# Performance work log

Hardware: AMD Instinct MI355X
Metric: run time of the kernel (lower is better)

The kernel has to match this reference:

```python
import jax, jax.numpy as jnp
import numpy as np

B, IN_CH, OUT_CH, N_MAPS, H, W_DIM, CTRL = 64, 32, 32, 64, 64, 64, 512
NF = N_MAPS                # forget gate units
NI = IN_CH * N_MAPS       # input gate units
NO = OUT_CH * N_MAPS      # output gate units


def setup_inputs() -> dict:
    key = jax.random.key(0)
    k1, k2, k3, k4 = jax.random.split(key, 4)
    inputs = jax.random.normal(k1, (B, IN_CH, H, W_DIM), dtype=jnp.float32)
    state = jax.random.normal(k2, (B, N_MAPS, H, W_DIM), dtype=jnp.float32)
    controls = jax.random.normal(k3, (B, CTRL), dtype=jnp.float32)
    Wc = jax.random.normal(k4, (NF + NI + NO, CTRL), dtype=jnp.float32) * (CTRL ** -0.5)
    return {"inputs": inputs, "state": state, "controls": controls, "W": Wc}


def reference(inputs, state, controls, W):
    # control linear (no bias): [B, NF+NI+NO]
    ctrl = controls @ W.T
    f = ctrl[:, :NF]                         # [B, n_maps]
    i = ctrl[:, NF:NF + NI]                  # [B, in_ch*n_maps]
    o = ctrl[:, NF + NI:]                    # [B, out_ch*n_maps]
    in_gates = i.reshape(B, N_MAPS, IN_CH)   # per-sample 1x1 conv filters
    forget_gates = f.reshape(B, N_MAPS, 1, 1)
    out_gates = o.reshape(B, OUT_CH, N_MAPS)
    # per-sample 1x1 conv == batched channel contraction
    gated_inputs = jnp.einsum('bchw,bmc->bmhw', inputs, in_gates)
    new_state = gated_inputs + state * forget_gates
    output = jnp.tanh(new_state)
    outputs = jnp.einsum('bmhw,bom->bohw', output, out_gates)
    return (outputs, new_state)
```

## Files before the change

kernel.cpp:

```cpp
#include <hip/hip_runtime.h>
#include <cstdint>
#include <cstddef>

#define B_SZ   64
#define IN_CH  32
#define OUT_CH 32
#define NMAPS  64
#define HW     4096
#define CTRLN  512
#define NROWS  4160
#define OUT0_SZ (B_SZ*OUT_CH*HW)
#define TILE   128

typedef short bf8_t  __attribute__((ext_vector_type(8)));
typedef float f32x4  __attribute__((ext_vector_type(4)));

__device__ __forceinline__ unsigned short f2bf(float f) {
    union { float f; uint32_t u; } v; v.f = f;
    return (unsigned short)((v.u + 0x7FFFu + ((v.u >> 16) & 1u)) >> 16);
}
__device__ __forceinline__ float fast_tanh(float x) {
    float e = __expf(2.0f * x);
    return 1.0f - 2.0f * __builtin_amdgcn_rcpf(e + 1.0f);
}

__global__ __launch_bounds__(256) void ctrl_gemm(
    const float* __restrict__ controls, const float* __restrict__ W,
    float* __restrict__ ws)
{
    __shared__ __align__(16) float ct[128 * 65];
    const int tid = threadIdx.x;
    const int b   = tid & 63;
    const int w   = __builtin_amdgcn_readfirstlane(tid >> 6);
    const int j0  = blockIdx.x * 16 + w * 4;
    const float* w0 = W + (size_t)j0 * CTRLN;

    float acc[4] = {0.f, 0.f, 0.f, 0.f};
    for (int kc = 0; kc < CTRLN; kc += 128) {
        __syncthreads();
#pragma unroll
        for (int i = 0; i < 8; ++i) {
            const int flat = (i * 256 + tid) * 4;
            const int bb = flat >> 7;
            const int kk = flat & 127;
            float4 v = *(const float4*)(controls + (size_t)bb * CTRLN + kc + kk);
            ct[(kk + 0) * 65 + bb] = v.x;
            ct[(kk + 1) * 65 + bb] = v.y;
            ct[(kk + 2) * 65 + bb] = v.z;
            ct[(kk + 3) * 65 + bb] = v.w;
        }
        __syncthreads();
#pragma unroll 4
        for (int k = 0; k < 128; ++k) {
            const float c = ct[k * 65 + b];
#pragma unroll
            for (int r = 0; r < 4; ++r)
                acc[r] += w0[r * CTRLN + kc + k] * c;
        }
    }
    float* wb = ws + (size_t)b * NROWS + j0;
#pragma unroll
    for (int r = 0; r < 4; ++r) wb[r] = acc[r];
}

__global__ __launch_bounds__(256, 4) void vstm_main(
    const float* __restrict__ inputs, const float* __restrict__ state,
    const float* __restrict__ ws, float* __restrict__ out)
{
    __shared__ __align__(16) unsigned short Xt[TILE * 40];
    __shared__ __align__(16) unsigned short IGs[64 * 40];
    __shared__ __align__(16) unsigned short OGs[32 * 72];
    __shared__ __align__(16) unsigned short Tt[TILE * 72];
    __shared__ __align__(16) float fs[64];

    const int tid  = threadIdx.x;
    const int b    = blockIdx.y;
    const int tile = blockIdx.x * TILE;
    const int w    = __builtin_amdgcn_readfirstlane(tid >> 6);
    const int l    = tid & 63;
    const int lhi  = l >> 4;
    const int llo  = l & 15;

    const float* g = ws + (size_t)b * NROWS;
    if (tid < 64) fs[tid] = g[tid];
#pragma unroll
    for (int i = 0; i < 8; ++i) {
        const int idx = i * 256 + tid;
        IGs[(idx >> 5) * 40 + (idx & 31)] = f2bf(g[64 + idx]);
        OGs[(idx >> 6) * 72 + (idx & 63)] = f2bf(g[2112 + idx]);
    }
    const float* inb = inputs + (size_t)b * IN_CH * HW + tile;
#pragma unroll
    for (int i = 0; i < 16; ++i) {
        const int flat = i * 256 + tid;
        const int c = flat >> 7, p = flat & 127;
        Xt[p * 40 + c] = f2bf(inb[c * HW + p]);
    }
    __syncthreads();

    const bf8_t af = *(const bf8_t*)&IGs[(w * 16 + llo) * 40 + lhi * 8];
    f32x4 acc[8];
#pragma unroll
    for (int pc = 0; pc < 8; ++pc) {
        acc[pc] = (f32x4){0.f, 0.f, 0.f, 0.f};
        const bf8_t bf = *(const bf8_t*)&Xt[(pc * 16 + llo) * 40 + lhi * 8];
        acc[pc] = __builtin_amdgcn_mfma_f32_16x16x32_bf16(af, bf, acc[pc], 0, 0, 0);
    }

    float fr[4];
#pragma unroll
    for (int r = 0; r < 4; ++r) fr[r] = fs[w * 16 + lhi * 4 + r];

    const float* stb = state + (size_t)b * NMAPS * HW + tile;
    float*       nsb = out + OUT0_SZ + (size_t)b * NMAPS * HW + tile;
#pragma unroll
    for (int pc = 0; pc < 8; ++pc) {
        const int p = pc * 16 + llo;
#pragma unroll
        for (int r = 0; r < 4; ++r) {
            const int m = w * 16 + lhi * 4 + r;
            const float ns = acc[pc][r] + stb[m * HW + p] * fr[r];
            nsb[m * HW + p] = ns;
            Tt[p * 72 + m] = f2bf(fast_tanh(ns));
        }
    }
    __syncthreads();

    const int oc  = w >> 1;
    const int pcb = (w & 1) * 4;
    bf8_t ag[2];
#pragma unroll
    for (int ks = 0; ks < 2; ++ks)
        ag[ks] = *(const bf8_t*)&OGs[(oc * 16 + llo) * 72 + ks * 32 + lhi * 8];

    f32x4 acc2[4];
#pragma unroll
    for (int t = 0; t < 4; ++t) {
        acc2[t] = (f32x4){0.f, 0.f, 0.f, 0.f};
        const int pc = pcb + t;
#pragma unroll
        for (int ks = 0; ks < 2; ++ks) {
            const bf8_t bt = *(const bf8_t*)&Tt[(pc * 16 + llo) * 72 + ks * 32 + lhi * 8];
            acc2[t] = __builtin_amdgcn_mfma_f32_16x16x32_bf16(ag[ks], bt, acc2[t], 0, 0, 0);
        }
    }

    float* ob = out + (size_t)b * OUT_CH * HW + tile;
#pragma unroll
    for (int t = 0; t < 4; ++t) {
        const int p = (pcb + t) * 16 + llo;
#pragma unroll
        for (int r = 0; r < 4; ++r) {
            const int o = oc * 16 + lhi * 4 + r;
            ob[o * HW + p] = acc2[t][r];
        }
    }
}

extern "C" void kernel_launch(void* const* d_in, const int* in_sizes, int n_in,
                              void* d_out, int out_size, void* d_ws, size_t ws_size,
                              hipStream_t stream) {
    const float* inputs   = (const float*)d_in[0];
    const float* state    = (const float*)d_in[1];
    const float* controls = (const float*)d_in[2];
    const float* W        = (const float*)d_in[3];
    float*       out      = (float*)d_out;
    float*       ws       = (float*)d_ws;

    ctrl_gemm<<<dim3(NROWS / 16), 256, 0, stream>>>(controls, W, ws);

    dim3 g2(HW / TILE, B_SZ);
    vstm_main<<<g2, 256, 0, stream>>>(inputs, state, ws, out);
}
```

Before: 227.8 us.

## Swap MFMA operand roles so each wave owns pixel rows and uses float4 state and output I/O

The main kernel swaps the MFMA A and B operands so each wave owns a 32-pixel slice across all maps. The accumulator rows then map to consecutive pixels, which lets state loads, new_state stores and output stores use float4 accesses. Because each wave only reads back its own Tt rows, the barrier between the tanh store and the second GEMM is removed. Gate staging is also vectorized to float4 loads, and the control GEMM is split into twice as many blocks with two rows per wave to raise parallelism. Removing the barrier relies on the same wave writing and then reading those Tt rows, and the transposed Tt stores stay scalar and may cause LDS bank conflicts.

```diff
diff --git a/kernel.cpp b/kernel.cpp
--- a/kernel.cpp
+++ b/kernel.cpp
@@ -13,6 +13,7 @@
 #define TILE   128
 
 typedef short bf8_t  __attribute__((ext_vector_type(8)));
+typedef short bf4_t  __attribute__((ext_vector_type(4)));
 typedef float f32x4  __attribute__((ext_vector_type(4)));
 
 __device__ __forceinline__ unsigned short f2bf(float f) {
@@ -32,10 +33,10 @@
     const int tid = threadIdx.x;
     const int b   = tid & 63;
     const int w   = __builtin_amdgcn_readfirstlane(tid >> 6);
-    const int j0  = blockIdx.x * 16 + w * 4;
+    const int j0  = blockIdx.x * 8 + w * 2;
     const float* w0 = W + (size_t)j0 * CTRLN;
 
-    float acc[4] = {0.f, 0.f, 0.f, 0.f};
+    float acc0 = 0.f, acc1 = 0.f;
     for (int kc = 0; kc < CTRLN; kc += 128) {
         __syncthreads();
 #pragma unroll
@@ -50,17 +51,15 @@
             ct[(kk + 3) * 65 + bb] = v.w;
         }
         __syncthreads();
-#pragma unroll 4
+#pragma unroll 8
         for (int k = 0; k < 128; ++k) {
             const float c = ct[k * 65 + b];
-#pragma unroll
-            for (int r = 0; r < 4; ++r)
-                acc[r] += w0[r * CTRLN + kc + k] * c;
-        }
-    }
-    float* wb = ws + (size_t)b * NROWS + j0;
-#pragma unroll
-    for (int r = 0; r < 4; ++r) wb[r] = acc[r];
+            acc0 += w0[kc + k] * c;
+            acc1 += w0[CTRLN + kc + k] * c;
+        }
+    }
+    ws[(size_t)b * NROWS + j0]     = acc0;
+    ws[(size_t)b * NROWS + j0 + 1] = acc1;
 }
 
 __global__ __launch_bounds__(256, 4) void vstm_main(
@@ -78,16 +77,22 @@
     const int tile = blockIdx.x * TILE;
     const int w    = __builtin_amdgcn_readfirstlane(tid >> 6);
     const int l    = tid & 63;
-    const int lhi  = l >> 4;
-    const int llo  = l & 15;
+    const int quad = l >> 4;
+    const int mlo  = l & 15;
 
     const float* g = ws + (size_t)b * NROWS;
     if (tid < 64) fs[tid] = g[tid];
 #pragma unroll
-    for (int i = 0; i < 8; ++i) {
-        const int idx = i * 256 + tid;
-        IGs[(idx >> 5) * 40 + (idx & 31)] = f2bf(g[64 + idx]);
-        OGs[(idx >> 6) * 72 + (idx & 63)] = f2bf(g[2112 + idx]);
+    for (int i = 0; i < 2; ++i) {
+        const int e = (i * 256 + tid) * 4;
+        float4 gi = *(const float4*)(g + 64 + e);
+        bf4_t vi = { (short)f2bf(gi.x), (short)f2bf(gi.y),
+                     (short)f2bf(gi.z), (short)f2bf(gi.w) };
+        *(bf4_t*)&IGs[(e >> 5) * 40 + (e & 31)] = vi;
+        float4 go = *(const float4*)(g + 2112 + e);
+        bf4_t vo = { (short)f2bf(go.x), (short)f2bf(go.y),
+                     (short)f2bf(go.z), (short)f2bf(go.w) };
+        *(bf4_t*)&OGs[(e >> 6) * 72 + (e & 63)] = vo;
     }
     const float* inb = inputs + (size_t)b * IN_CH * HW + tile;
 #pragma unroll
@@ -98,63 +103,85 @@
     }
     __syncthreads();
 
-    const bf8_t af = *(const bf8_t*)&IGs[(w * 16 + llo) * 40 + lhi * 8];
-    f32x4 acc[8];
-#pragma unroll
-    for (int pc = 0; pc < 8; ++pc) {
-        acc[pc] = (f32x4){0.f, 0.f, 0.f, 0.f};
-        const bf8_t bf = *(const bf8_t*)&Xt[(pc * 16 + llo) * 40 + lhi * 8];
-        acc[pc] = __builtin_amdgcn_mfma_f32_16x16x32_bf16(af, bf, acc[pc], 0, 0, 0);
-    }
-
-    float fr[4];
-#pragma unroll
-    for (int r = 0; r < 4; ++r) fr[r] = fs[w * 16 + lhi * 4 + r];
+    bf8_t af[2], bg[4];
+#pragma unroll
+    for (int pc = 0; pc < 2; ++pc)
+        af[pc] = *(const bf8_t*)&Xt[(w * 32 + pc * 16 + mlo) * 40 + quad * 8];
+#pragma unroll
+    for (int mc = 0; mc < 4; ++mc)
+        bg[mc] = *(const bf8_t*)&IGs[(mc * 16 + mlo) * 40 + quad * 8];
+
+    f32x4 acc[2][4];
+#pragma unroll
+    for (int pc = 0; pc < 2; ++pc)
+#pragma unroll
+        for (int mc = 0; mc < 4; ++mc) {
+            acc[pc][mc] = (f32x4){0.f, 0.f, 0.f, 0.f};
+            acc[pc][mc] = __builtin_amdgcn_mfma_f32_16x16x32_bf16(
+                af[pc], bg[mc], acc[pc][mc], 0, 0, 0);
+        }
 
     const float* stb = state + (size_t)b * NMAPS * HW + tile;
     float*       nsb = out + OUT0_SZ + (size_t)b * NMAPS * HW + tile;
 #pragma unroll
-    for (int pc = 0; pc < 8; ++pc) {
-        const int p = pc * 16 + llo;
-#pragma unroll
-        for (int r = 0; r < 4; ++r) {
-            const int m = w * 16 + lhi * 4 + r;
-            const float ns = acc[pc][r] + stb[m * HW + p] * fr[r];
-            nsb[m * HW + p] = ns;
-            Tt[p * 72 + m] = f2bf(fast_tanh(ns));
-        }
-    }
-    __syncthreads();
-
-    const int oc  = w >> 1;
-    const int pcb = (w & 1) * 4;
-    bf8_t ag[2];
-#pragma unroll
-    for (int ks = 0; ks < 2; ++ks)
-        ag[ks] = *(const bf8_t*)&OGs[(oc * 16 + llo) * 72 + ks * 32 + lhi * 8];
-
-    f32x4 acc2[4];
-#pragma unroll
-    for (int t = 0; t < 4; ++t) {
-        acc2[t] = (f32x4){0.f, 0.f, 0.f, 0.f};
-        const int pc = pcb + t;
-#pragma unroll
-        for (int ks = 0; ks < 2; ++ks) {
-            const bf8_t bt = *(const bf8_t*)&Tt[(pc * 16 + llo) * 72 + ks * 32 + lhi * 8];
-            acc2[t] = __builtin_amdgcn_mfma_f32_16x16x32_bf16(ag[ks], bt, acc2[t], 0, 0, 0);
-        }
-    }
+    for (int mc = 0; mc < 4; ++mc) {
+        const int m = mc * 16 + mlo;
+        const float fgt = fs[m];
+#pragma unroll
+        for (int pc = 0; pc < 2; ++pc) {
+            const int p0 = w * 32 + pc * 16 + quad * 4;
+            const float4 st = *(const float4*)(stb + (size_t)m * HW + p0);
+            float4 ns;
+            ns.x = acc[pc][mc][0] + st.x * fgt;
+            ns.y = acc[pc][mc][1] + st.y * fgt;
+            ns.z = acc[pc][mc][2] + st.z * fgt;
+            ns.w = acc[pc][mc][3] + st.w * fgt;
+            *(float4*)(nsb + (size_t)m * HW + p0) = ns;
+            Tt[(p0 + 0) * 72 + m] = f2bf(fast_tanh(ns.x));
+            Tt[(p0 + 1) * 72 + m] = f2bf(fast_tanh(ns.y));
+            Tt[(p0 + 2) * 72 + m] = f2bf(fast_tanh(ns.z));
+            Tt[(p0 + 3) * 72 + m] = f2bf(fast_tanh(ns.w));
+        }
+    }
+
+    bf8_t ag[2][2], at[2][2];
+#pragma unroll
+    for (int oc = 0; oc < 2; ++oc)
+#pragma unroll
+        for (int ks = 0; ks < 2; ++ks)
+            ag[oc][ks] = *(const bf8_t*)&OGs[(oc * 16 + mlo) * 72 + ks * 32 + quad * 8];
+#pragma unroll
+    for (int pc = 0; pc < 2; ++pc)
+#pragma unroll
+        for (int ks = 0; ks < 2; ++ks)
+            at[pc][ks] = *(const bf8_t*)&Tt[(w * 32 + pc * 16 + mlo) * 72 + ks * 32 + quad * 8];
+
+    f32x4 acc2[2][2];
+#pragma unroll
+    for (int pc = 0; pc < 2; ++pc)
+#pragma unroll
+        for (int oc = 0; oc < 2; ++oc) {
+            acc2[pc][oc] = (f32x4){0.f, 0.f, 0.f, 0.f};
+#pragma unroll
+            for (int ks = 0; ks < 2; ++ks)
+                acc2[pc][oc] = __builtin_amdgcn_mfma_f32_16x16x32_bf16(
+                    at[pc][ks], ag[oc][ks], acc2[pc][oc], 0, 0, 0);
+        }
 
     float* ob = out + (size_t)b * OUT_CH * HW + tile;
 #pragma unroll
-    for (int t = 0; t < 4; ++t) {
-        const int p = (pcb + t) * 16 + llo;
-#pragma unroll
-        for (int r = 0; r < 4; ++r) {
-            const int o = oc * 16 + lhi * 4 + r;
-            ob[o * HW + p] = acc2[t][r];
-        }
-    }
+    for (int pc = 0; pc < 2; ++pc)
+#pragma unroll
+        for (int oc = 0; oc < 2; ++oc) {
+            const int p0 = w * 32 + pc * 16 + quad * 4;
+            const int o  = oc * 16 + mlo;
+            float4 r;
+            r.x = acc2[pc][oc][0];
+            r.y = acc2[pc][oc][1];
+            r.z = acc2[pc][oc][2];
+            r.w = acc2[pc][oc][3];
+            *(float4*)(ob + (size_t)o * HW + p0) = r;
+        }
 }
 
 extern "C" void kernel_launch(void* const* d_in, const int* in_sizes, int n_in,
@@ -167,7 +194,7 @@
     float*       out      = (float*)d_out;
     float*       ws       = (float*)d_ws;
 
-    ctrl_gemm<<<dim3(NROWS / 16), 256, 0, stream>>>(controls, W, ws);
+    ctrl_gemm<<<dim3(NROWS / 8), 256, 0, stream>>>(controls, W, ws);
 
     dim3 g2(HW / TILE, B_SZ);
     vstm_main<<<g2, 256, 0, stream>>>(inputs, state, ws, out);
```

Result: no change. 224.7 us (-1.4%).
